# Optimization experiments

Hardware: AMD Instinct MI355X
Metric: run time of the kernel (lower is better)

The kernel has to match this reference:

```python
import jax, jax.numpy as jnp
import numpy as np

# Module hyperparameters (from init_kwargs)
IN_C = 64
OUT_C = 64
K = 3
STRIDE = 1
PAD = 1
DIL = 1
OVERLAP = 4
CENTER_SIZE = 4

# Input sizes
B, H, W = 16, 128, 128


def _crop_mask(h, w):
    """Static (trace-time) crop mask: zeros on the central crop window, ones elsewhere.

    Matches the intended semantics of CropConv's python-loop mask: rows
    [crop_start, crop_start+crop_size) x cols [crop_start, crop_start+crop_size)
    of the HxW output grid are zeroed.
    """
    crop_start = (h - h // CENTER_SIZE) // 2 - OVERLAP  # 44 for h=128
    crop_size = h // CENTER_SIZE + 2 * OVERLAP          # 40 for h=128
    m = np.ones((h, w), dtype=np.float32)
    m[crop_start:crop_start + crop_size, crop_start:crop_start + crop_size] = 0.0
    return jnp.asarray(m)


def setup_inputs() -> dict:
    key = jax.random.key(0)
    kx, kw = jax.random.split(key)
    x = jax.random.normal(kx, (B, IN_C, H, W), dtype=jnp.float32)
    # kaiming_normal_ fan_out init: std = sqrt(2 / (out_channels * k * k))
    w_std = np.sqrt(2.0 / (OUT_C * K * K)).astype(np.float32)
    weight = jax.random.normal(kw, (OUT_C, IN_C, K, K), dtype=jnp.float32) * w_std
    return {"x": x, "weight": weight}


def reference(x, weight):
    # im2col (Unfold) + matmul == a standard dense conv; use the fused conv primitive.
    out = jax.lax.conv_general_dilated(
        x, weight,
        window_strides=(STRIDE, STRIDE),
        padding=((PAD, PAD), (PAD, PAD)),
        rhs_dilation=(DIL, DIL),
        dimension_numbers=("NCHW", "OIHW", "NCHW"),
    )  # [B, OUT_C, H, W] (same-size conv)
    mask = _crop_mask(out.shape[2], out.shape[3])  # [H, W], {0,1}
    # torch.where(mask, out, 0) == out * mask (mask is constant wrt grads)
    return out * mask
```

## Files before the change

### kernel.cpp

```cpp
#include <hip/hip_runtime.h>
#include <stdint.h>


#define B_ 16
#define C_ 64
#define H_ 128
#define W_ 128

#define XLDS_U4 4096

typedef float f32x4 __attribute__((ext_vector_type(4)));
typedef short bf16x8 __attribute__((ext_vector_type(8)));

__device__ inline unsigned short f2bf(float f) {
    union { float f; uint32_t u; } v; v.f = f;
    uint32_t u = v.u + 0x7FFF + ((v.u >> 16) & 1);
    return (unsigned short)(u >> 16);
}

__global__ __launch_bounds__(256) void xform_weight(
    const float* __restrict__ wgt, uint16_t* __restrict__ Wb)
{
    int L = blockIdx.x * 256 + threadIdx.x;
    int e    = L & 7;
    int lane = (L >> 3) & 63;
    int i    = (L >> 9) & 3;
    int ch   = (L >> 11) & 1;
    int kk   = L >> 12;
    int oc   = i * 16 + (lane & 15);
    int ic   = ch * 32 + (lane >> 4) * 8 + e;
    Wb[L] = f2bf(wgt[((size_t)oc * 64 + ic) * 9 + kk]);
}

__global__ __launch_bounds__(256, 2) void conv_main(
    const uint4* __restrict__ Wq,
    const float* __restrict__ x,
    float* __restrict__ out)
{
    __shared__ uint4 lds[XLDS_U4];

    const int t    = threadIdx.x;
    const int lane = t & 63;
    const int wv   = t >> 6;
    const int n    = lane & 15;
    const int q    = lane >> 4;

    const int d    = blockIdx.x;
    const int orig = (d & 7) * 128 + (d >> 3);
    const int b    = orig >> 6;
    const int h0   = (orig & 63) * 2;

    {
        const int c     = t & 127;
        const int jbase = (t >> 7) * 4;
        #pragma unroll
        for (int r = 0; r < 4; ++r) {
            const int h = h0 - 1 + r;
            if (h < 0 || h >= H_) {
                uint4 z; z.x = z.y = z.z = z.w = 0;
                #pragma unroll
                for (int jj = 0; jj < 4; ++jj)
                    lds[r * 1024 + c * 8 + ((jbase + jj + c) & 7)] = z;
            } else {
                const float* src = x + (((size_t)b * C_) * H_ + h) * W_ + c;
                #pragma unroll
                for (int jj = 0; jj < 4; ++jj) {
                    const int j = jbase + jj;
                    uint32_t u[4];
                    #pragma unroll
                    for (int p = 0; p < 4; ++p) {
                        float v0 = src[(size_t)(j * 8 + 2 * p)     * (H_ * W_)];
                        float v1 = src[(size_t)(j * 8 + 2 * p + 1) * (H_ * W_)];
                        u[p] = (uint32_t)f2bf(v0) | ((uint32_t)f2bf(v1) << 16);
                    }
                    lds[r * 1024 + c * 8 + ((j + c) & 7)] =
                        *(const uint4*)u;
                }
            }
        }
    }
    __syncthreads();

    f32x4 acc[4][4];
    #pragma unroll
    for (int i = 0; i < 4; ++i)
        #pragma unroll
        for (int tt = 0; tt < 4; ++tt)
            acc[i][tt] = (f32x4){0.f, 0.f, 0.f, 0.f};

    const int wb = (wv & 1) * 64;
    const bool lz = (wb + n) == 0;
    const bool rz = (wb + n) == 79;
    const bf16x8 zfrag = 0;

    #pragma unroll
    for (int kh = 0; kh < 3; ++kh) {
        const int row = (wv >> 1) + kh;
        #pragma unroll
        for (int kw = 0; kw < 3; ++kw) {
            const int kk = kh * 3 + kw;
            #pragma unroll
            for (int ch = 0; ch < 2; ++ch) {
                bf16x8 a[4], bb[4];
                #pragma unroll
                for (int i = 0; i < 4; ++i)
                    a[i] = __builtin_bit_cast(bf16x8,
                        Wq[((kk * 2 + ch) * 4 + i) * 64 + lane]);
                #pragma unroll
                for (int tt = 0; tt < 4; ++tt) {
                    int c   = wb + tt * 16 + n + kw - 1;
                    int cc  = min(max(c, 0), 127);
                    int idx = (row * 128 + cc) * 8 + ((ch * 4 + q + cc) & 7);
                    bf16x8 v = __builtin_bit_cast(bf16x8, lds[idx]);
                    if (kw == 0 && tt == 0) v = lz ? zfrag : v;
                    if (kw == 2 && tt == 3) v = rz ? zfrag : v;
                    bb[tt] = v;
                }
                #pragma unroll
                for (int i = 0; i < 4; ++i)
                    #pragma unroll
                    for (int tt = 0; tt < 4; ++tt)
                        acc[i][tt] = __builtin_amdgcn_mfma_f32_16x16x32_bf16(
                            a[i], bb[tt], acc[i][tt], 0, 0, 0);
            }
        }
    }

    const int  h  = h0 + (wv >> 1);
    const bool hz = (h >= 44 && h < 84);
    #pragma unroll
    for (int i = 0; i < 4; ++i) {
        #pragma unroll
        for (int tt = 0; tt < 4; ++tt) {
            const int  w0 = wb + tt * 16 + n;
            const bool zz = hz && (w0 >= 44 && w0 < 84);
            #pragma unroll
            for (int r = 0; r < 4; ++r) {
                const int oc = i * 16 + q * 4 + r;
                out[(((size_t)b * C_ + oc) * H_ + h) * W_ + w0] =
                    zz ? 0.f : acc[i][tt][r];
            }
        }
    }
}

#define WLDS_U4 4608

__global__ __launch_bounds__(256, 1) void conv_fused(
    const float* __restrict__ x,
    const float* __restrict__ wgt,
    float* __restrict__ out)
{
    __shared__ uint4 lds[WLDS_U4 + XLDS_U4];
    uint16_t* lds16 = (uint16_t*)lds;

    const int t    = threadIdx.x;
    const int lane = t & 63;
    const int wv   = t >> 6;
    const int n    = lane & 15;
    const int q    = lane >> 4;

    const int d    = blockIdx.x;
    const int orig = (d & 7) * 128 + (d >> 3);
    const int b    = orig >> 6;
    const int h0   = (orig & 63) * 2;

    #pragma unroll
    for (int p = 0; p < 2; ++p) {
        const int a_  = t + 256 * p;
        const int oc  = a_ >> 3;
        const int oct = a_ & 7;
        const float* src = wgt + (size_t)oc * 576 + (size_t)oct * 72;
        f32x4 w4[18];
        #pragma unroll
        for (int j = 0; j < 18; ++j) w4[j] = ((const f32x4*)src)[j];
        const int ch = oct >> 2, qq = oct & 3;
        const int ii = oc >> 4,  nn = oc & 15;
        #pragma unroll
        for (int kk = 0; kk < 9; ++kk) {
            #define WELEM(e) ((uint32_t)f2bf(w4[((e)*9 + kk) >> 2][((e)*9 + kk) & 3]))
            uint4 val;
            val.x = WELEM(0) | (WELEM(1) << 16);
            val.y = WELEM(2) | (WELEM(3) << 16);
            val.z = WELEM(4) | (WELEM(5) << 16);
            val.w = WELEM(6) | (WELEM(7) << 16);
            #undef WELEM
            lds[((kk * 2 + ch) * 4 + ii) * 64 + qq * 16 + nn] = val;
        }
    }

    {
        const int ic    = t >> 2;
        const int w0    = (t & 3) * 32;
        const int jslot = ic >> 3;
        const int esub  = ic & 7;
        #pragma unroll
        for (int r = 0; r < 4; ++r) {
            const int h = h0 - 1 + r;
            if (h < 0 || h >= H_) {
                uint4 z; z.x = z.y = z.z = z.w = 0;
                #pragma unroll
                for (int k = 0; k < 4; ++k)
                    lds[WLDS_U4 + r * 1024 + k * 256 + t] = z;
            } else {
                const float* src =
                    x + (((size_t)(b * C_ + ic)) * H_ + h) * W_ + w0;
                f32x4 v4[8];
                #pragma unroll
                for (int j = 0; j < 8; ++j) v4[j] = ((const f32x4*)src)[j];
                #pragma unroll
                for (int k = 0; k < 32; ++k) {
                    const int c    = w0 + k;
                    const int slot = (jslot + c) & 7;
                    lds16[WLDS_U4 * 8 + ((r * 128 + c) * 8 + slot) * 8 + esub] =
                        f2bf(v4[k >> 2][k & 3]);
                }
            }
        }
    }
    __syncthreads();

    f32x4 acc[4][4];
    #pragma unroll
    for (int i = 0; i < 4; ++i)
        #pragma unroll
        for (int tt = 0; tt < 4; ++tt)
            acc[i][tt] = (f32x4){0.f, 0.f, 0.f, 0.f};

    const int wb = (wv & 1) * 64;
    const uint4* Wl = lds;
    const uint4* Xl = lds + WLDS_U4;
    const bool lz = (wb + n) == 0;
    const bool rz = (wb + n) == 79;
    const bf16x8 zfrag = 0;

    #pragma unroll
    for (int kh = 0; kh < 3; ++kh) {
        const int row = (wv >> 1) + kh;
        #pragma unroll
        for (int kw = 0; kw < 3; ++kw) {
            const int kk = kh * 3 + kw;
            #pragma unroll
            for (int ch = 0; ch < 2; ++ch) {
                bf16x8 a[4], bb[4];
                #pragma unroll
                for (int i = 0; i < 4; ++i)
                    a[i] = __builtin_bit_cast(bf16x8,
                        Wl[((kk * 2 + ch) * 4 + i) * 64 + lane]);
                #pragma unroll
                for (int tt = 0; tt < 4; ++tt) {
                    int c   = wb + tt * 16 + n + kw - 1;
                    int cc  = min(max(c, 0), 127);
                    int idx = (row * 128 + cc) * 8 + ((ch * 4 + q + cc) & 7);
                    bf16x8 v = __builtin_bit_cast(bf16x8, Xl[idx]);
                    if (kw == 0 && tt == 0) v = lz ? zfrag : v;
                    if (kw == 2 && tt == 3) v = rz ? zfrag : v;
                    bb[tt] = v;
                }
                #pragma unroll
                for (int i = 0; i < 4; ++i)
                    #pragma unroll
                    for (int tt = 0; tt < 4; ++tt)
                        acc[i][tt] = __builtin_amdgcn_mfma_f32_16x16x32_bf16(
                            a[i], bb[tt], acc[i][tt], 0, 0, 0);
            }
        }
    }

    const int  h  = h0 + (wv >> 1);
    const bool hz = (h >= 44 && h < 84);
    #pragma unroll
    for (int i = 0; i < 4; ++i) {
        #pragma unroll
        for (int tt = 0; tt < 4; ++tt) {
            const int  w0 = wb + tt * 16 + n;
            const bool zz = hz && (w0 >= 44 && w0 < 84);
            #pragma unroll
            for (int r = 0; r < 4; ++r) {
                const int oc = i * 16 + q * 4 + r;
                out[(((size_t)b * C_ + oc) * H_ + h) * W_ + w0] =
                    zz ? 0.f : acc[i][tt][r];
            }
        }
    }
}

extern "C" void kernel_launch(void* const* d_in, const int* in_sizes, int n_in,
                              void* d_out, int out_size, void* d_ws, size_t ws_size,
                              hipStream_t stream) {
    const float* x   = (const float*)d_in[0];
    const float* wgt = (const float*)d_in[1];
    float* out       = (float*)d_out;

    const size_t W_BYTES = 9 * 2 * 4 * 64 * 16;
    if (ws_size >= W_BYTES) {
        uint16_t* Wb = (uint16_t*)d_ws;
        xform_weight<<<dim3(144), dim3(256), 0, stream>>>(wgt, Wb);
        conv_main<<<dim3(1024), dim3(256), 0, stream>>>(
            (const uint4*)Wb, x, out);
    } else {
        conv_fused<<<dim3(1024), dim3(256), 0, stream>>>(x, wgt, out);
    }
}
```

Before: 132.5 us.

## Retile conv_main to 4x64 output tiles with halo columns in LDS

Changes each conv_main block from a 2-row by 128-column output tile to a 4-row by 64-column tile with a 6x66 halo-padded input tile in LDS. Explicit halo columns remove the clamp/zero-select logic from the inner loop, and the smaller LDS footprint lets launch bounds request 3 blocks per CU instead of 2. The trade-off is more redundant input loading per output, since vertical halo overhead is now 6 rows for 4 outputs instead of 4 for 2, plus column halo loads with scattered strided gathers.

```diff
diff --git a/kernel.cpp b/kernel.cpp
--- a/kernel.cpp
+++ b/kernel.cpp
@@ -7,7 +7,9 @@
 #define H_ 128
 #define W_ 128
 
-#define XLDS_U4 4096
+#define TROWS 6
+#define TCOLS 66
+#define XLDS_U4 (TROWS * TCOLS * 8)
 
 typedef float f32x4 __attribute__((ext_vector_type(4)));
 typedef short bf16x8 __attribute__((ext_vector_type(8)));
@@ -32,7 +34,7 @@
     Wb[L] = f2bf(wgt[((size_t)oc * 64 + ic) * 9 + kk]);
 }
 
-__global__ __launch_bounds__(256, 2) void conv_main(
+__global__ __launch_bounds__(256, 3) void conv_main(
     const uint4* __restrict__ Wq,
     const float* __restrict__ x,
     float* __restrict__ out)
@@ -47,25 +49,30 @@
 
     const int d    = blockIdx.x;
     const int orig = (d & 7) * 128 + (d >> 3);
+    const int wsd  = orig & 1;
+    const int ht   = (orig >> 1) & 31;
     const int b    = orig >> 6;
-    const int h0   = (orig & 63) * 2;
+    const int h0   = ht * 4;
 
     {
-        const int c     = t & 127;
-        const int jbase = (t >> 7) * 4;
-        #pragma unroll
-        for (int r = 0; r < 4; ++r) {
+        const int cc_   = (t & 63) + 1;
+        const int jh    = (t >> 6) & 1;
+        const int rtri  = (t >> 7) * 3;
+        const int wglob = wsd * 64 + (t & 63);
+        #pragma unroll
+        for (int rr = 0; rr < 3; ++rr) {
+            const int r = rtri + rr;
             const int h = h0 - 1 + r;
             if (h < 0 || h >= H_) {
                 uint4 z; z.x = z.y = z.z = z.w = 0;
                 #pragma unroll
                 for (int jj = 0; jj < 4; ++jj)
-                    lds[r * 1024 + c * 8 + ((jbase + jj + c) & 7)] = z;
+                    lds[(r * TCOLS + cc_) * 8 + ((jh * 4 + jj + cc_) & 7)] = z;
             } else {
-                const float* src = x + (((size_t)b * C_) * H_ + h) * W_ + c;
+                const float* src = x + (((size_t)b * C_) * H_ + h) * W_ + wglob;
                 #pragma unroll
                 for (int jj = 0; jj < 4; ++jj) {
-                    const int j = jbase + jj;
+                    const int j = jh * 4 + jj;
                     uint32_t u[4];
                     #pragma unroll
                     for (int p = 0; p < 4; ++p) {
@@ -73,10 +80,29 @@
                         float v1 = src[(size_t)(j * 8 + 2 * p + 1) * (H_ * W_)];
                         u[p] = (uint32_t)f2bf(v0) | ((uint32_t)f2bf(v1) << 16);
                     }
-                    lds[r * 1024 + c * 8 + ((j + c) & 7)] =
-                        *(const uint4*)u;
-                }
-            }
+                    lds[(r * TCOLS + cc_) * 8 + ((j + cc_) & 7)] = *(const uint4*)u;
+                }
+            }
+        }
+        if (t < 96) {
+            const int j  = t & 7;
+            const int r  = (t >> 3) % 6;
+            const int ce = (t >= 48) ? (TCOLS - 1) : 0;
+            const int h  = h0 - 1 + r;
+            const int wg = wsd * 64 + ce - 1;
+            uint4 val; val.x = val.y = val.z = val.w = 0;
+            if (h >= 0 && h < H_ && wg >= 0 && wg < W_) {
+                const float* src = x + (((size_t)b * C_) * H_ + h) * W_ + wg;
+                uint32_t u[4];
+                #pragma unroll
+                for (int p = 0; p < 4; ++p) {
+                    float v0 = src[(size_t)(j * 8 + 2 * p)     * (H_ * W_)];
+                    float v1 = src[(size_t)(j * 8 + 2 * p + 1) * (H_ * W_)];
+                    u[p] = (uint32_t)f2bf(v0) | ((uint32_t)f2bf(v1) << 16);
+                }
+                val = *(const uint4*)u;
+            }
+            lds[(r * TCOLS + ce) * 8 + ((j + ce) & 7)] = val;
         }
     }
     __syncthreads();
@@ -85,17 +111,14 @@
     #pragma unroll
     for (int i = 0; i < 4; ++i)
         #pragma unroll
-        for (int tt = 0; tt < 4; ++tt)
-            acc[i][tt] = (f32x4){0.f, 0.f, 0.f, 0.f};
-
-    const int wb = (wv & 1) * 64;
-    const bool lz = (wb + n) == 0;
-    const bool rz = (wb + n) == 79;
-    const bf16x8 zfrag = 0;
+        for (int f = 0; f < 4; ++f)
+            acc[i][f] = (f32x4){0.f, 0.f, 0.f, 0.f};
+
+    const int wbh   = (wv & 1) * 32;
+    const int hbase = (wv >> 1) * 2;
 
     #pragma unroll
     for (int kh = 0; kh < 3; ++kh) {
-        const int row = (wv >> 1) + kh;
         #pragma unroll
         for (int kw = 0; kw < 3; ++kw) {
             const int kk = kh * 3 + kw;
@@ -107,51 +130,50 @@
                     a[i] = __builtin_bit_cast(bf16x8,
                         Wq[((kk * 2 + ch) * 4 + i) * 64 + lane]);
                 #pragma unroll
-                for (int tt = 0; tt < 4; ++tt) {
-                    int c   = wb + tt * 16 + n + kw - 1;
-                    int cc  = min(max(c, 0), 127);
-                    int idx = (row * 128 + cc) * 8 + ((ch * 4 + q + cc) & 7);
-                    bf16x8 v = __builtin_bit_cast(bf16x8, lds[idx]);
-                    if (kw == 0 && tt == 0) v = lz ? zfrag : v;
-                    if (kw == 2 && tt == 3) v = rz ? zfrag : v;
-                    bb[tt] = v;
+                for (int f = 0; f < 4; ++f) {
+                    const int hh  = f >> 1, tt = f & 1;
+                    const int row = hbase + hh + kh;
+                    const int ct  = wbh + tt * 16 + n + kw;
+                    const int idx = (row * TCOLS + ct) * 8 + ((ch * 4 + q + ct) & 7);
+                    bb[f] = __builtin_bit_cast(bf16x8, lds[idx]);
                 }
                 #pragma unroll
                 for (int i = 0; i < 4; ++i)
                     #pragma unroll
-                    for (int tt = 0; tt < 4; ++tt)
-                        acc[i][tt] = __builtin_amdgcn_mfma_f32_16x16x32_bf16(
-                            a[i], bb[tt], acc[i][tt], 0, 0, 0);
-            }
-        }
-    }
-
-    const int  h  = h0 + (wv >> 1);
-    const bool hz = (h >= 44 && h < 84);
-    #pragma unroll
-    for (int i = 0; i < 4; ++i) {
-        #pragma unroll
-        for (int tt = 0; tt < 4; ++tt) {
-            const int  w0 = wb + tt * 16 + n;
-            const bool zz = hz && (w0 >= 44 && w0 < 84);
+                    for (int f = 0; f < 4; ++f)
+                        acc[i][f] = __builtin_amdgcn_mfma_f32_16x16x32_bf16(
+                            a[i], bb[f], acc[i][f], 0, 0, 0);
+            }
+        }
+    }
+
+    #pragma unroll
+    for (int f = 0; f < 4; ++f) {
+        const int hh = f >> 1, tt = f & 1;
+        const int h  = h0 + hbase + hh;
+        const int w0 = wsd * 64 + wbh + tt * 16 + n;
+        const bool zz = (h >= 44 && h < 84) && (w0 >= 44 && w0 < 84);
+        #pragma unroll
+        for (int i = 0; i < 4; ++i) {
             #pragma unroll
             for (int r = 0; r < 4; ++r) {
                 const int oc = i * 16 + q * 4 + r;
                 out[(((size_t)b * C_ + oc) * H_ + h) * W_ + w0] =
-                    zz ? 0.f : acc[i][tt][r];
+                    zz ? 0.f : acc[i][f][r];
             }
         }
     }
 }
 
 #define WLDS_U4 4608
+#define FXLDS_U4 4096
 
 __global__ __launch_bounds__(256, 1) void conv_fused(
     const float* __restrict__ x,
     const float* __restrict__ wgt,
     float* __restrict__ out)
 {
-    __shared__ uint4 lds[WLDS_U4 + XLDS_U4];
+    __shared__ uint4 lds[WLDS_U4 + FXLDS_U4];
     uint16_t* lds16 = (uint16_t*)lds;
 
     const int t    = threadIdx.x;
```

New measurement: 130.6 us. Within noise of the previous version (-1.5%).
